# Kernel optimization log

Hardware: AMD Instinct MI355X
Metric: run time of the kernel (lower is better)

Reference implementation:

```python
import jax, jax.numpy as jnp
import numpy as np

LEAK = 0.01  # F.leaky_relu default negative_slope
TAU = 1.0    # sinkhorn_tau
ITERS = 5    # sinkhorn_iters


def leaky_relu(x):
    return jnp.where(x >= 0, x, LEAK * x)


def setup_inputs() -> dict:
    key = jax.random.key(0)
    B, N, F, E, H, L = 512, 200, 32, 128, 128, 2
    ks = jax.random.split(key, 8)
    def s(k, shape, fan_in):
        return jax.random.normal(k, shape, dtype=jnp.float32) * (1.0 / np.sqrt(fan_in)).astype(np.float32)
    return {
        "x": jax.random.normal(ks[0], (B, N, F), dtype=jnp.float32),
        "w_emb": s(ks[1], (E, F), F),
        "b_emb": jnp.zeros((E,), jnp.float32),
        "w_ih": s(ks[2], (L, 4 * H, E), H),   # stacked per-layer LSTM input weights
        "w_hh": s(ks[3], (L, 4 * H, H), H),   # stacked per-layer LSTM recurrent weights
        "b_ih": jnp.zeros((L, 4 * H), jnp.float32),
        "b_hh": jnp.zeros((L, 4 * H), jnp.float32),
        "w_fc1": s(ks[4], (E, H), H),
        "b_fc1": jnp.zeros((E,), jnp.float32),
        "w_fc2": s(ks[5], (N, E), E),
        "b_fc2": jnp.zeros((N,), jnp.float32),
        "do_round": 0,  # non-differentiable Hungarian rounding path disabled
    }


def _lstm_layer(xs, h0, c0, Wih, Whh, b):
    # xs: [N, B, E]  (seq-major, like torch.nn.LSTM); h0, c0: [B, H]
    def step(carry, x_t):
        h, c = carry
        g = x_t @ Wih.T + h @ Whh.T + b               # [B, 4H]
        i, f, gg, o = jnp.split(g, 4, axis=-1)        # torch gate order i,f,g,o
        c = jax.nn.sigmoid(f) * c + jax.nn.sigmoid(i) * jnp.tanh(gg)
        h = jax.nn.sigmoid(o) * jnp.tanh(c)
        return (h, c), h
    (hN, cN), hs = jax.lax.scan(step, (h0, c0), xs)
    return hs, hN, cN


def _sinkhorn(M, tau, n_iters):
    # exp(M / tau) followed by alternating row / column normalization
    x = jnp.exp(M / tau)
    for _ in range(n_iters):
        x = x / jnp.sum(x, axis=2, keepdims=True)  # row normalize
        x = x / jnp.sum(x, axis=1, keepdims=True)  # column normalize
    return x


def reference(x, w_emb, b_emb, w_ih, w_hh, b_ih, b_hh, w_fc1, b_fc1, w_fc2, b_fc2, do_round):
    # do_round=0: the Hungarian rounding branch (host round-trip) is skipped;
    # the module then returns just the Sinkhorn output psi.
    B = x.shape[0]
    H = w_hh.shape[-1]
    e = leaky_relu(x @ w_emb.T + b_emb)            # [B, N, E]
    xs = jnp.transpose(e, (1, 0, 2))               # [N, B, E]
    h = jnp.zeros((B, H), x.dtype)
    c = jnp.zeros((B, H), x.dtype)
    hs = xs
    # NB: original code feeds the SAME embedded x to every LSTM layer,
    # carrying only the (h, c) state between layers.
    for l in range(w_ih.shape[0]):
        hs, h, c = _lstm_layer(xs, h, c, w_ih[l], w_hh[l], b_ih[l] + b_hh[l])
    out = jnp.transpose(hs, (1, 0, 2))             # [B, N, H]
    out = leaky_relu(out @ w_fc1.T + b_fc1)        # [B, N, E]
    M = out @ w_fc2.T + b_fc2                      # [B, N, N]
    psi = _sinkhorn(M, TAU, ITERS)
    return psi
```

## Files before the change

### kernel.cpp

```cpp
#include <hip/hip_runtime.h>
#include <cstdint>
#include <cstddef>

#define LEAK 0.01f
#define L2E 1.4426950408889634f

typedef _Float16 f16;
typedef __attribute__((ext_vector_type(4))) _Float16 f16x4;
typedef __attribute__((ext_vector_type(8))) _Float16 f16x8;
typedef __attribute__((ext_vector_type(4))) float f32x4;

static __device__ __forceinline__ f16x8 pack8s(float4 a, float4 b, float s) {
  f16x8 r;
  r[0] = (f16)(a.x * s); r[1] = (f16)(a.y * s); r[2] = (f16)(a.z * s); r[3] = (f16)(a.w * s);
  r[4] = (f16)(b.x * s); r[5] = (f16)(b.y * s); r[6] = (f16)(b.z * s); r[7] = (f16)(b.w * s);
  return r;
}
static __device__ __forceinline__ f16x8 pack8(float4 a, float4 b) {
  return pack8s(a, b, 1.0f);
}
#define MFMA16(a, b, c) __builtin_amdgcn_mfma_f32_16x16x32_f16((a), (b), (c), 0, 0, 0)

__constant__ float SCG[4] = {L2E, L2E, 2.0f * L2E, L2E};

__global__ __launch_bounds__(256) void k_emb(
    const float* __restrict__ x, const float* __restrict__ wemb,
    const float* __restrict__ bemb, f16* __restrict__ e) {
  const int t = blockIdx.x, tid = threadIdx.x;
  __shared__ __align__(16) float wl[128 * 32];
  __shared__ float bl[128];
  for (int idx = tid; idx < 1024; idx += 256)
    ((float4*)wl)[idx] = ((const float4*)wemb)[idx];
  if (tid < 128) bl[tid] = bemb[tid];

  float xa[32], xb[32];
  const float* xpa = x + ((size_t)tid * 200 + t) * 32;
  const float* xpb = x + ((size_t)(tid + 256) * 200 + t) * 32;
#pragma unroll
  for (int k4 = 0; k4 < 8; ++k4) {
    float4 va = *(const float4*)(xpa + k4 * 4);
    float4 vb = *(const float4*)(xpb + k4 * 4);
    xa[k4 * 4 + 0] = va.x; xa[k4 * 4 + 1] = va.y; xa[k4 * 4 + 2] = va.z; xa[k4 * 4 + 3] = va.w;
    xb[k4 * 4 + 0] = vb.x; xb[k4 * 4 + 1] = vb.y; xb[k4 * 4 + 2] = vb.z; xb[k4 * 4 + 3] = vb.w;
  }
  __syncthreads();

  f16* ea = e + ((size_t)t * 512 + tid) * 128;
  f16* eb = e + ((size_t)t * 512 + tid + 256) * 128;
  for (int j8 = 0; j8 < 16; ++j8) {
    f16x8 oa, ob;
#pragma unroll
    for (int jj = 0; jj < 8; ++jj) {
      int j = j8 * 8 + jj;
      float aa = bl[j], ab = bl[j];
#pragma unroll
      for (int k4 = 0; k4 < 8; ++k4) {
        float4 wv = *(const float4*)&wl[j * 32 + k4 * 4];
        aa += xa[k4 * 4 + 0] * wv.x + xa[k4 * 4 + 1] * wv.y +
              xa[k4 * 4 + 2] * wv.z + xa[k4 * 4 + 3] * wv.w;
        ab += xb[k4 * 4 + 0] * wv.x + xb[k4 * 4 + 1] * wv.y +
              xb[k4 * 4 + 2] * wv.z + xb[k4 * 4 + 3] * wv.w;
      }
      oa[jj] = (f16)(aa >= 0.f ? aa : LEAK * aa);
      ob[jj] = (f16)(ab >= 0.f ? ab : LEAK * ab);
    }
    *(f16x8*)(ea + j8 * 8) = oa;
    *(f16x8*)(eb + j8 * 8) = ob;
  }
}

static __device__ __forceinline__ void xp_waves(
    const f16* __restrict__ e, const float* __restrict__ wih,
    const float* __restrict__ bih, const float* __restrict__ bhh,
    f16* __restrict__ xp, int t0, int wid, int nrep, int stride, int lane) {
  const int q = lane >> 4, l16 = lane & 15;
  const int ct = wid & 7;

  f16x8 BW[4][4];
  float bias[4];
#pragma unroll
  for (int G = 0; G < 4; ++G) {
    int n = G * 128 + ct * 16 + l16;
    bias[G] = (bih[n] + bhh[n]) * SCG[G];
#pragma unroll
    for (int kc = 0; kc < 4; ++kc) {
      const float4* p = (const float4*)(wih + (size_t)n * 128 + kc * 32 + q * 8);
      BW[G][kc] = pack8s(p[0], p[1], SCG[G]);
    }
  }
  for (int rep = 0; rep < nrep; ++rep) {
    int task = wid + rep * stride;
    int g2 = task >> 3;
    int tl = g2 >> 2, btg = g2 & 3;
#pragma unroll
    for (int p = 0; p < 8; ++p) {
      int bt = btg * 8 + p;
      const f16* A = e + ((size_t)(t0 + tl) * 512 + bt * 16 + l16) * 128 + q * 8;
      f16x8 af[4];
#pragma unroll
      for (int kc = 0; kc < 4; ++kc) af[kc] = *(const f16x8*)(A + kc * 32);
      f32x4 acc[4];
#pragma unroll
      for (int G = 0; G < 4; ++G)
        acc[G] = (f32x4){bias[G], bias[G], bias[G], bias[G]};
#pragma unroll
      for (int kc = 0; kc < 4; ++kc)
#pragma unroll
        for (int G = 0; G < 4; ++G)
          acc[G] = MFMA16(af[kc], BW[G][kc], acc[G]);
      f16x8 oA, oB;
#pragma unroll
      for (int r = 0; r < 4; ++r) {
        oA[r]     = (f16)acc[0][r];
        oA[4 + r] = (f16)acc[1][r];
        oB[r]     = (f16)acc[2][r];
        oB[4 + r] = (f16)acc[3][r];
      }
      f16* dst = xp + (size_t)tl * 262144 + bt * 8192 + ct * 1024 + lane * 16;
      *(f16x8*)dst = oA;
      *(f16x8*)(dst + 8) = oB;
    }
  }
}

__global__ __launch_bounds__(256, 2) void k_xp(
    const f16* __restrict__ e, const float* __restrict__ wih,
    const float* __restrict__ bih, const float* __restrict__ bhh,
    f16* __restrict__ xp, int t0) {
  xp_waves(e, wih, bih, bhh, xp, t0,
           blockIdx.x * 4 + (threadIdx.x >> 6), 1, 0, threadIdx.x & 63);
}

static __device__ __forceinline__ void rec_body(
    const f16* __restrict__ xp, const float* __restrict__ whh,
    float* __restrict__ hws, float* __restrict__ cws,
    f16* __restrict__ hs, int layer, int t0, int CH, int bt) {
  const int tid = threadIdx.x;
  const int w = tid >> 6, lane = tid & 63, q = lane >> 4, l16 = lane & 15;
  __shared__ __align__(16) f16 hlds[2][16][136];

  f16x8 BH[4][4];
#pragma unroll
  for (int G = 0; G < 4; ++G) {
    int n = G * 128 + w * 16 + l16;
#pragma unroll
    for (int kc = 0; kc < 4; ++kc) {
      const float4* ph = (const float4*)(whh + (size_t)n * 128 + kc * 32 + q * 8);
      BH[G][kc] = pack8s(ph[0], ph[1], SCG[G]);
    }
  }

  f32x4 cst;
  if (layer == 0 && t0 == 0) {
    cst = (f32x4){0.f, 0.f, 0.f, 0.f};
    for (int idx = tid; idx < 2 * 16 * 136; idx += 512)
      ((f16*)hlds)[idx] = (f16)0.f;
  } else {
    cst = *(const f32x4*)(cws + ((size_t)(bt * 8 + w) * 64 + lane) * 4);
    f32x4 hv = *(const f32x4*)(hws + ((size_t)(bt * 8 + w) * 64 + lane) * 4);
#pragma unroll
    for (int r = 0; r < 4; ++r)
      hlds[1][q * 4 + r][w * 16 + l16] = (f16)hv[r];
  }
  __syncthreads();

  const f16* xpl = xp + (((size_t)bt * 8 + w) * 64 + lane) * 16;
  f16x8 xa = *(const f16x8*)(xpl);
  f16x8 xb = *(const f16x8*)(xpl + 8);

  f32x4 hk;
  const int srow = tid >> 5, scol = (tid & 31) * 4;
  for (int tl = 0; tl < CH; ++tl) {
    int tn = (tl + 1 < CH) ? tl + 1 : tl;
    const f16* xpn = xpl + (size_t)tn * 262144;
    f16x8 nxa = *(const f16x8*)(xpn);
    f16x8 nxb = *(const f16x8*)(xpn + 8);

    const int rb = (tl + 1) & 1;
    f16x8 ah[4];
#pragma unroll
    for (int kc = 0; kc < 4; ++kc)
      ah[kc] = *(const f16x8*)&hlds[rb][l16][kc * 32 + q * 8];

    f32x4 acc[4];
#pragma unroll
    for (int r = 0; r < 4; ++r) {
      acc[0][r] = (float)xa[r];
      acc[1][r] = (float)xa[4 + r];
      acc[2][r] = (float)xb[r];
      acc[3][r] = (float)xb[4 + r];
    }
#pragma unroll
    for (int kc = 0; kc < 4; ++kc)
#pragma unroll
      for (int G = 0; G < 4; ++G)
        acc[G] = MFMA16(ah[kc], BH[G][kc], acc[G]);

    const int wb = tl & 1;
#pragma unroll
    for (int r = 0; r < 4; ++r) {
      float ui = __builtin_amdgcn_exp2f(-acc[0][r]);
      float uf = __builtin_amdgcn_exp2f(-acc[1][r]);
      float ug = __builtin_amdgcn_exp2f(-fmaxf(acc[2][r], -88.f));
      float uo = __builtin_amdgcn_exp2f(-acc[3][r]);
      float sf = __builtin_amdgcn_rcpf(1.0f + uf);
      float p1 = (1.0f - ug) * __builtin_amdgcn_rcpf((1.0f + ui) * (1.0f + ug));
      float cc = sf * cst[r] + p1;
      cst[r] = cc;
      float ccl = fminf(fmaxf(cc, -30.f), 30.f) * (-2.0f * L2E);
      float ucc = __builtin_amdgcn_exp2f(ccl);
      float hv = (1.0f - ucc) * __builtin_amdgcn_rcpf((1.0f + uo) * (1.0f + ucc));
      hk[r] = hv;
      hlds[wb][q * 4 + r][w * 16 + l16] = (f16)hv;
    }
    __syncthreads();
    if (layer != 0) {
      f16x4 hv4 = *(const f16x4*)&hlds[wb][srow][scol];
      *(f16x4*)(hs + ((size_t)(bt * 16 + srow) * 200 + (t0 + tl)) * 128 + scol) = hv4;
    }
    xa = nxa; xb = nxb;
  }

  *(f32x4*)(hws + ((size_t)(bt * 8 + w) * 64 + lane) * 4) = hk;
  *(f32x4*)(cws + ((size_t)(bt * 8 + w) * 64 + lane) * 4) = cst;
}

__global__ __launch_bounds__(512, 2) void k_rec(
    const f16* __restrict__ xp, const float* __restrict__ whh,
    float* __restrict__ hws, float* __restrict__ cws,
    f16* __restrict__ hs, int layer, int t0, int CH) {
  rec_body(xp, whh, hws, cws, hs, layer, t0, CH, blockIdx.x);
}

__global__ __launch_bounds__(512, 2) void k_recxp(
    const f16* __restrict__ xp_r, const float* __restrict__ whh,
    float* __restrict__ hws, float* __restrict__ cws,
    f16* __restrict__ hs, int layer, int t0_r,
    const f16* __restrict__ e, const float* __restrict__ wih_n,
    const float* __restrict__ bih_n, const float* __restrict__ bhh_n,
    f16* __restrict__ xp_w, int t0_x) {
  if (blockIdx.x < 32) {
    rec_body(xp_r, whh, hws, cws, hs, layer, t0_r, 100, blockIdx.x);
  } else {
    xp_waves(e, wih_n, bih_n, bhh_n, xp_w, t0_x,
             (blockIdx.x - 32) * 8 + (threadIdx.x >> 6), 2, 1600,
             threadIdx.x & 63);
  }
}

__global__ __launch_bounds__(256, 2) void k_head(
    const f16* __restrict__ hs, const float* __restrict__ wfc1,
    const float* __restrict__ bfc1, const float* __restrict__ wfc2,
    const float* __restrict__ bfc2, float* __restrict__ psi) {
  extern __shared__ char smem[];
  f16* E = (f16*)smem;
  f16* o1 = (f16*)(smem + 27200);
  float* uu = (float*)(smem + 80000);
  float* vv = (float*)(smem + 80800);
  const int b = blockIdx.x, tid = threadIdx.x;
  const int w = tid >> 6, lane = tid & 63, q = lane >> 4, l16 = lane & 15;
  const f16* A = hs + (size_t)b * 200 * 128;

  f16x8 BF1[2][4];
  float bias1[2];
#pragma unroll
  for (int s = 0; s < 2; ++s) {
    int n = w * 32 + s * 16 + l16;
    bias1[s] = bfc1[n];
#pragma unroll
    for (int kc = 0; kc < 4; ++kc) {
      const float4* p = (const float4*)(wfc1 + (size_t)n * 128 + kc * 32 + q * 8);
      BF1[s][kc] = pack8(p[0], p[1]);
    }
  }
  f16x8 BF2[4][4];
  float bias2[4] = {0.f, 0.f, 0.f, 0.f};
#pragma unroll
  for (int ci = 0; ci < 4; ++ci) {
    int ct = w + ci * 4;
    if (ct < 13) {
      int n = ct * 16 + l16; if (n > 199) n = 199;
      bias2[ci] = bfc2[n];
#pragma unroll
      for (int kc = 0; kc < 4; ++kc) {
        const float4* p = (const float4*)(wfc2 + (size_t)n * 128 + kc * 32 + q * 8);
        BF2[ci][kc] = pack8(p[0], p[1]);
      }
    }
  }

  for (int rt = 0; rt < 13; ++rt) {
    int m = rt * 16 + l16; if (m > 199) m = 199;
    f16x8 af[4];
#pragma unroll
    for (int kc = 0; kc < 4; ++kc)
      af[kc] = *(const f16x8*)(A + (size_t)m * 128 + kc * 32 + q * 8);
#pragma unroll
    for (int s = 0; s < 2; ++s) {
      f32x4 acc = (f32x4){bias1[s], bias1[s], bias1[s], bias1[s]};
#pragma unroll
      for (int kc = 0; kc < 4; ++kc) acc = MFMA16(af[kc], BF1[s][kc], acc);
      int col = w * 32 + s * 16 + l16;
#pragma unroll
      for (int r = 0; r < 4; ++r) {
        int row = rt * 16 + q * 4 + r;
        float vvv = acc[r]; vvv = vvv >= 0.f ? vvv : LEAK * vvv;
        if (row < 200) o1[row * 136 + col] = (f16)vvv;
      }
    }
  }
  __syncthreads();

  for (int rt = 0; rt < 13; ++rt) {
    int m = rt * 16 + l16; if (m > 199) m = 199;
    f16x8 af[4];
#pragma unroll
    for (int kc = 0; kc < 4; ++kc)
      af[kc] = *(const f16x8*)&o1[m * 136 + kc * 32 + q * 8];
    __syncthreads();
#pragma unroll
    for (int ci = 0; ci < 4; ++ci) {
      int ct = w + ci * 4;
      if (ct < 13) {
        f32x4 acc = (f32x4){bias2[ci], bias2[ci], bias2[ci], bias2[ci]};
#pragma unroll
        for (int kc = 0; kc < 4; ++kc) acc = MFMA16(af[kc], BF2[ci][kc], acc);
        int col = ct * 16 + l16;
#pragma unroll
        for (int r = 0; r < 4; ++r) {
          int row = rt * 16 + q * 4 + r;
          if (row < 200 && col < 200) E[row * 200 + col] = (f16)__expf(acc[r]);
        }
      }
    }
  }
  __syncthreads();
  if (tid < 200) vv[tid] = 1.0f;
  __syncthreads();

  for (int it = 0; it < 5; ++it) {
    if (tid < 200) {
      const f16* Er = E + tid * 200;
      float s0 = 0.f, s1 = 0.f;
      for (int j = 0; j < 200; j += 4) {
        f16x4 e4 = *(const f16x4*)(Er + j);
        float4 v4 = *(const float4*)(vv + j);
        s0 += (float)e4[0] * v4.x + (float)e4[1] * v4.y;
        s1 += (float)e4[2] * v4.z + (float)e4[3] * v4.w;
      }
      uu[tid] = __builtin_amdgcn_rcpf(s0 + s1);
    }
    __syncthreads();
    if (tid < 200) {
      float s0 = 0.f, s1 = 0.f;
      for (int i = 0; i < 200; i += 4) {
        float4 u4 = *(const float4*)(uu + i);
        s0 += (float)E[(i + 0) * 200 + tid] * u4.x + (float)E[(i + 1) * 200 + tid] * u4.y;
        s1 += (float)E[(i + 2) * 200 + tid] * u4.z + (float)E[(i + 3) * 200 + tid] * u4.w;
      }
      vv[tid] = __builtin_amdgcn_rcpf(s0 + s1);
    }
    __syncthreads();
  }

  float* P = psi + (size_t)b * 40000;
  for (int idx4 = tid; idx4 < 10000; idx4 += 256) {
    unsigned i = ((unsigned)idx4 * 5243u) >> 18;
    unsigned jq = (unsigned)idx4 - i * 50u;
    f16x4 e4 = *(const f16x4*)(E + i * 200 + jq * 4);
    float4 v4 = *(const float4*)(vv + jq * 4);
    float ui = uu[i];
    float4 o;
    o.x = ui * (float)e4[0] * v4.x;
    o.y = ui * (float)e4[1] * v4.y;
    o.z = ui * (float)e4[2] * v4.z;
    o.w = ui * (float)e4[3] * v4.w;
    *(float4*)(P + i * 200 + jq * 4) = o;
  }
}

extern "C" void kernel_launch(void* const* d_in, const int* in_sizes, int n_in,
                              void* d_out, int out_size, void* d_ws, size_t ws_size,
                              hipStream_t stream) {
  const float* x    = (const float*)d_in[0];
  const float* wemb = (const float*)d_in[1];
  const float* bemb = (const float*)d_in[2];
  const float* wih  = (const float*)d_in[3];
  const float* whh  = (const float*)d_in[4];
  const float* bih  = (const float*)d_in[5];
  const float* bhh  = (const float*)d_in[6];
  const float* wfc1 = (const float*)d_in[7];
  const float* bfc1 = (const float*)d_in[8];
  const float* wfc2 = (const float*)d_in[9];
  const float* bfc2 = (const float*)d_in[10];
  float* psi = (float*)d_out;

  char* ws = (char*)d_ws;
  f16*   e   = (f16*)(ws);
  float* hws = (float*)(ws + 26214400);
  float* cws = (float*)(ws + 26476544);
  f16*   hs  = (f16*)(ws + 26738688);
  f16*   xpA = (f16*)(ws + 52953088);
  f16*   xpB = (f16*)(ws + 105381888);

  const size_t fixed = 52953088;
  const bool pipelined = (ws_size >= 157810688ull);

  (void)hipFuncSetAttribute((const void*)k_head,
                            hipFuncAttributeMaxDynamicSharedMemorySize, 81600);

  k_emb<<<200, 256, 0, stream>>>(x, wemb, bemb, e);

  const float* wih1 = wih + 65536;  const float* whh1 = whh + 65536;
  const float* bih1 = bih + 512;    const float* bhh1 = bhh + 512;

  if (pipelined) {
    k_xp<<<800, 256, 0, stream>>>(e, wih, bih, bhh, xpA, 0);
    k_recxp<<<232, 512, 0, stream>>>(xpA, whh, hws, cws, hs, 0, 0,
                                     e, wih, bih, bhh, xpB, 100);
    k_recxp<<<232, 512, 0, stream>>>(xpB, whh, hws, cws, hs, 0, 100,
                                     e, wih1, bih1, bhh1, xpA, 0);
    k_recxp<<<232, 512, 0, stream>>>(xpA, whh1, hws, cws, hs, 1, 0,
                                     e, wih1, bih1, bhh1, xpB, 100);
    k_rec<<<32, 512, 0, stream>>>(xpB, whh1, hws, cws, hs, 1, 100, 100);
  } else {
    const int cands[] = {100, 50, 40, 25, 20, 10, 8, 5, 4, 2, 1};
    int CH = 1;
    for (int ci = 0; ci < 11; ++ci) {
      if (fixed + (size_t)cands[ci] * 524288 <= ws_size) { CH = cands[ci]; break; }
    }
    for (int l = 0; l < 2; ++l) {
      const float* wih_l = wih + (size_t)l * 65536;
      const float* whh_l = whh + (size_t)l * 65536;
      const float* bih_l = bih + (size_t)l * 512;
      const float* bhh_l = bhh + (size_t)l * 512;
      for (int t0 = 0; t0 < 200; t0 += CH) {
        k_xp<<<CH * 8, 256, 0, stream>>>(e, wih_l, bih_l, bhh_l, xpA, t0);
        k_rec<<<32, 512, 0, stream>>>(xpA, whh_l, hws, cws, hs, l, t0, CH);
      }
    }
  }
  k_head<<<512, 256, 81600, stream>>>(hs, wfc1, bfc1, wfc2, bfc2, psi);
}
```

Measured before the change: 619.0 us.

## Widen head kernel to 512 threads and parallelize Sinkhorn reductions

The head kernel now runs with 512 threads (8 waves) instead of 256. The FC1 and FC2 column tiles are redistributed so each wave owns fewer tiles. The Sinkhorn row sums split each row across two threads, and the column sums are restructured so 8 threads each cover a group of 25 rows for 4 adjacent columns, combined with shuffle reductions. This puts 400 of the 512 threads to work in the Sinkhorn loop, where previously only 200 were busy, and the column pass reads 4 contiguous f16 values per load instead of scattered scalars. The tradeoff is extra shuffle work, and the 81.6KB of shared memory per block still caps occupancy, so the launch bound of 4 blocks per CU may not be met.

```diff
diff --git a/kernel.cpp b/kernel.cpp
--- a/kernel.cpp
+++ b/kernel.cpp
@@ -248,7 +248,7 @@
   }
 }
 
-__global__ __launch_bounds__(256, 2) void k_head(
+__global__ __launch_bounds__(512, 4) void k_head(
     const f16* __restrict__ hs, const float* __restrict__ wfc1,
     const float* __restrict__ bfc1, const float* __restrict__ wfc2,
     const float* __restrict__ bfc2, float* __restrict__ psi) {
@@ -261,23 +261,22 @@
   const int w = tid >> 6, lane = tid & 63, q = lane >> 4, l16 = lane & 15;
   const f16* A = hs + (size_t)b * 200 * 128;
 
-  f16x8 BF1[2][4];
-  float bias1[2];
-#pragma unroll
-  for (int s = 0; s < 2; ++s) {
-    int n = w * 32 + s * 16 + l16;
-    bias1[s] = bfc1[n];
+  f16x8 BF1[4];
+  float bias1;
+  {
+    int n = w * 16 + l16;
+    bias1 = bfc1[n];
 #pragma unroll
     for (int kc = 0; kc < 4; ++kc) {
       const float4* p = (const float4*)(wfc1 + (size_t)n * 128 + kc * 32 + q * 8);
-      BF1[s][kc] = pack8(p[0], p[1]);
-    }
-  }
-  f16x8 BF2[4][4];
-  float bias2[4] = {0.f, 0.f, 0.f, 0.f};
-#pragma unroll
-  for (int ci = 0; ci < 4; ++ci) {
-    int ct = w + ci * 4;
+      BF1[kc] = pack8(p[0], p[1]);
+    }
+  }
+  f16x8 BF2[2][4];
+  float bias2[2] = {0.f, 0.f};
+#pragma unroll
+  for (int ci = 0; ci < 2; ++ci) {
+    int ct = w + ci * 8;
     if (ct < 13) {
       int n = ct * 16 + l16; if (n > 199) n = 199;
       bias2[ci] = bfc2[n];
@@ -295,18 +294,15 @@
 #pragma unroll
     for (int kc = 0; kc < 4; ++kc)
       af[kc] = *(const f16x8*)(A + (size_t)m * 128 + kc * 32 + q * 8);
-#pragma unroll
-    for (int s = 0; s < 2; ++s) {
-      f32x4 acc = (f32x4){bias1[s], bias1[s], bias1[s], bias1[s]};
-#pragma unroll
-      for (int kc = 0; kc < 4; ++kc) acc = MFMA16(af[kc], BF1[s][kc], acc);
-      int col = w * 32 + s * 16 + l16;
-#pragma unroll
-      for (int r = 0; r < 4; ++r) {
-        int row = rt * 16 + q * 4 + r;
-        float vvv = acc[r]; vvv = vvv >= 0.f ? vvv : LEAK * vvv;
-        if (row < 200) o1[row * 136 + col] = (f16)vvv;
-      }
+    f32x4 acc = (f32x4){bias1, bias1, bias1, bias1};
+#pragma unroll
+    for (int kc = 0; kc < 4; ++kc) acc = MFMA16(af[kc], BF1[kc], acc);
+    int col = w * 16 + l16;
+#pragma unroll
+    for (int r = 0; r < 4; ++r) {
+      int row = rt * 16 + q * 4 + r;
+      float vvv = acc[r]; vvv = vvv >= 0.f ? vvv : LEAK * vvv;
+      if (row < 200) o1[row * 136 + col] = (f16)vvv;
     }
   }
   __syncthreads();
@@ -319,8 +315,8 @@
       af[kc] = *(const f16x8*)&o1[m * 136 + kc * 32 + q * 8];
     __syncthreads();
 #pragma unroll
-    for (int ci = 0; ci < 4; ++ci) {
-      int ct = w + ci * 4;
+    for (int ci = 0; ci < 2; ++ci) {
+      int ct = w + ci * 8;
       if (ct < 13) {
         f32x4 acc = (f32x4){bias2[ci], bias2[ci], bias2[ci], bias2[ci]};
 #pragma unroll
@@ -339,32 +335,55 @@
   __syncthreads();
 
   for (int it = 0; it < 5; ++it) {
-    if (tid < 200) {
-      const f16* Er = E + tid * 200;
+    if (tid < 400) {
+      int r = tid >> 1, h = tid & 1;
+      const f16* Er = E + r * 200 + h * 100;
+      const float* vp = vv + h * 100;
       float s0 = 0.f, s1 = 0.f;
-      for (int j = 0; j < 200; j += 4) {
+      for (int j = 0; j < 100; j += 4) {
         f16x4 e4 = *(const f16x4*)(Er + j);
-        float4 v4 = *(const float4*)(vv + j);
+        float4 v4 = *(const float4*)(vp + j);
         s0 += (float)e4[0] * v4.x + (float)e4[1] * v4.y;
         s1 += (float)e4[2] * v4.z + (float)e4[3] * v4.w;
       }
-      uu[tid] = __builtin_amdgcn_rcpf(s0 + s1);
+      float s = s0 + s1;
+      s += __shfl_xor(s, 1);
+      if (h == 0) uu[r] = __builtin_amdgcn_rcpf(s);
     }
     __syncthreads();
-    if (tid < 200) {
-      float s0 = 0.f, s1 = 0.f;
-      for (int i = 0; i < 200; i += 4) {
-        float4 u4 = *(const float4*)(uu + i);
-        s0 += (float)E[(i + 0) * 200 + tid] * u4.x + (float)E[(i + 1) * 200 + tid] * u4.y;
-        s1 += (float)E[(i + 2) * 200 + tid] * u4.z + (float)E[(i + 3) * 200 + tid] * u4.w;
-      }
-      vv[tid] = __builtin_amdgcn_rcpf(s0 + s1);
+    if (tid < 400) {
+      int c4 = tid >> 3, g = tid & 7;
+      const f16* Ec = E + (size_t)(g * 25) * 200 + c4 * 4;
+      float a0 = 0.f, a1 = 0.f, a2 = 0.f, a3 = 0.f;
+      for (int i = 0; i < 25; ++i) {
+        f16x4 e4 = *(const f16x4*)(Ec + i * 200);
+        float ui = uu[g * 25 + i];
+        a0 += (float)e4[0] * ui;
+        a1 += (float)e4[1] * ui;
+        a2 += (float)e4[2] * ui;
+        a3 += (float)e4[3] * ui;
+      }
+#pragma unroll
+      for (int mk = 1; mk <= 4; mk <<= 1) {
+        a0 += __shfl_xor(a0, mk);
+        a1 += __shfl_xor(a1, mk);
+        a2 += __shfl_xor(a2, mk);
+        a3 += __shfl_xor(a3, mk);
+      }
+      if (g == 0) {
+        float4 o;
+        o.x = __builtin_amdgcn_rcpf(a0);
+        o.y = __builtin_amdgcn_rcpf(a1);
+        o.z = __builtin_amdgcn_rcpf(a2);
+        o.w = __builtin_amdgcn_rcpf(a3);
+        *(float4*)(vv + c4 * 4) = o;
+      }
     }
     __syncthreads();
   }
 
   float* P = psi + (size_t)b * 40000;
-  for (int idx4 = tid; idx4 < 10000; idx4 += 256) {
+  for (int idx4 = tid; idx4 < 10000; idx4 += 512) {
     unsigned i = ((unsigned)idx4 * 5243u) >> 18;
     unsigned jq = (unsigned)idx4 - i * 50u;
     f16x4 e4 = *(const f16x4*)(E + i * 200 + jq * 4);
@@ -440,5 +459,5 @@
       }
     }
   }
-  k_head<<<512, 256, 81600, stream>>>(hs, wfc1, bfc1, wfc2, bfc2, psi);
-}
+  k_head<<<512, 512, 81600, stream>>>(hs, wfc1, bfc1, wfc2, bfc2, psi);
+}
```

Result: no change. 609.0 us (-1.6%).
